# Optimization experiments

Measured on AMD Instinct MI355X. Metric: run time of the kernel, lower is better.

## Reference

```python
import jax, jax.numpy as jnp
from jax import lax
import numpy as np

B, H, W_, C, F = 4, 32, 32, 16, 16
KH, KW = 3, 3
L = 1.0


def setup_inputs() -> dict:
    key = jax.random.key(0)
    k1, k2, k3, k4 = jax.random.split(key, 4)
    inputs = jax.random.normal(k1, (B, H, W_, C), dtype=jnp.float32)
    # lecun_normal-style scales (stddev = 1/sqrt(fan_in))
    m_scale = 1.0 / np.sqrt(H * W_ * 1)
    g_scale = 1.0 / np.sqrt(KH * KW * C)
    M = jax.random.normal(k2, (H, W_, 1, H, W_, 1), dtype=jnp.float32) * m_scale
    Wp = jax.random.normal(k3, (H, W_, 1, H, W_, 1), dtype=jnp.float32) * m_scale
    G = jax.random.normal(k4, (H, W_, KH, KW, C, F), dtype=jnp.float32) * g_scale
    return {"inputs": inputs, "M": M, "Wp": Wp, "G": G}


def reference(inputs, M, Wp, G):
    b, h, w, c = inputs.shape
    kh, kw, f = G.shape[2], G.shape[3], G.shape[5]
    M2 = M[:, :, 0, :, :, 0]   # (i,j,p,q)
    W2 = Wp[:, :, 0, :, :, 0]  # (i,j,p,q)
    # first_term[b,i,j,c] = sum_pq M[i,j,p,q] * inputs[b,p,q,c]
    first = jnp.einsum('ijpq,bpqc->bijc', M2, inputs)
    # One big conv: kernel (kh,kw,c, h*w*f) gives shifted for every output pixel (i,j)
    K = jnp.transpose(G, (2, 3, 4, 0, 1, 5)).reshape(kh, kw, c, h * w * f)
    shifted = lax.conv_general_dilated(
        inputs, K, window_strides=(1, 1), padding='SAME',
        dimension_numbers=('NHWC', 'HWIO', 'NHWC'))
    shifted = shifted.reshape(b, h, w, h, w, f)  # (b,p,q,i,j,f)
    diff = jax.nn.relu(inputs[:, :, :, None, None, :] - shifted)  # (b,p,q,i,j,c)
    # second_term[b,i,j,c] = sum_pq W[i,j,p,q] * relu(inputs - shifted)[b,p,q,i,j,c]
    second = jnp.einsum('ijpq,bpqijc->bijc', W2, diff)
    return first - L * second
```

## Files before the change

### kernel.cpp

```cpp
#include <hip/hip_runtime.h>


typedef __attribute__((ext_vector_type(8))) short bf16x8;
typedef __attribute__((ext_vector_type(4))) float f32x4;

__device__ inline unsigned short f2bf(float x) {
    unsigned u = __float_as_uint(x);
    u += 0x7FFFu + ((u >> 16) & 1u);
    return (unsigned short)(u >> 16);
}
__device__ inline unsigned pack2(float a, float b) {
    return (unsigned)f2bf(a) | ((unsigned)f2bf(b) << 16);
}

__global__ __launch_bounds__(256, 2) void inrf_fused(
    const float* __restrict__ inp,
    const float* __restrict__ M,
    const float* __restrict__ Wp,
    const float* __restrict__ G,
    float* __restrict__ out)
{
    const int bid = blockIdx.x;
    const int g = bid >> 2, b = bid & 3;
    const int t = threadIdx.x, w = t >> 6, l = t & 63;
    const int quad = l >> 4, m = l & 15;
    const int half = quad & 1;

    __shared__ __align__(16) uint4 Xl[1156 * 2];
    __shared__ __align__(16) short Gt[4 * 16 * 168];
    __shared__ float red[4][64];

    for (int i = t; i < 2312; i += 256) Xl[i] = (uint4){0, 0, 0, 0};
    for (int i = t; i < 1536; i += 256) {
        const int ij = i / 384, r2 = i - ij * 384;
        const int cf = r2 / 24, kp = r2 - cf * 24;
        Gt[(ij * 16 + cf) * 168 + 144 + kp] = 0;
    }
    for (int i = t; i < 9216; i += 256) {
        const int ij = i / 2304, r2 = i - ij * 2304;
        const int k = r2 >> 4, cf = r2 & 15;
        Gt[(ij * 16 + cf) * 168 + k] = (short)f2bf(G[g * 9216 + i]);
    }
    __syncthreads();

    {
        const float4* xb = (const float4*)(inp + b * 16384);
        for (int r = t; r < 1024; r += 256) {
            const int p = r >> 5, q = r & 31;
            const int hc = (p + 1) * 34 + (q + 1);
            const float4 f0 = xb[r * 4 + 0], f1 = xb[r * 4 + 1];
            const float4 f2 = xb[r * 4 + 2], f3 = xb[r * 4 + 3];
            uint4 lo, hi;
            lo.x = pack2(f0.x, f0.y); lo.y = pack2(f0.z, f0.w);
            lo.z = pack2(f1.x, f1.y); lo.w = pack2(f1.z, f1.w);
            hi.x = pack2(f2.x, f2.y); hi.y = pack2(f2.z, f2.w);
            hi.z = pack2(f3.x, f3.y); hi.w = pack2(f3.z, f3.w);
            const int sw = hc & 1;
            Xl[2 * hc + sw] = lo;
            Xl[2 * hc + (sw ^ 1)] = hi;
        }
    }

    bf16x8 Bf[4][5];
#pragma unroll
    for (int ij = 0; ij < 4; ++ij)
#pragma unroll
        for (int kk = 0; kk < 5; ++kk)
            Bf[ij][kk] = *(const bf16x8*)&Gt[(ij * 16 + m) * 168 + kk * 32 + quad * 8];

    int K_[5];
#pragma unroll
    for (int kk = 0; kk < 5; ++kk) {
        const int tap = 2 * kk + (quad >> 1);
        const int dh = tap / 3, dw = tap - dh * 3;
        K_[kk] = (dh * 34 + dw) * 32 + ((half ^ (dw & 1)) << 4);
    }
    __syncthreads();

    const int tile0w = w * 16;
    const float* wrow = Wp + g * 4096;
    const float* mrow = M + g * 4096;
    const float* xrow = inp + b * 16384 + m;

    auto loadA = [&](int i, uint4* dst) {
        const int pq = (tile0w + i) * 16 + m;
        const int p = pq >> 5, q = pq & 31;
        const int base = (p * 34 + q) * 32;
        const int qo = (q & 1) << 4;
#pragma unroll
        for (int kk = 0; kk < 5; ++kk) {
            int a = (base + K_[kk]) ^ qo;
            if (kk == 4) a = (quad >= 2) ? 0 : a;
            dst[kk] = *(const uint4*)((const char*)Xl + a);
        }
    };

    float accv[4] = {0.f, 0.f, 0.f, 0.f};
    uint4 Acur[5], Anxt[5];
    loadA(0, Acur);

    for (int i = 0; i < 16; ++i) {
        const int pqb = (tile0w + i) * 16 + quad * 4;

        float4 w2[4], m2[4];
        float xv[4];
#pragma unroll
        for (int ij = 0; ij < 4; ++ij) {
            w2[ij] = *(const float4*)&wrow[ij * 1024 + pqb];
            m2[ij] = *(const float4*)&mrow[ij * 1024 + pqb];
        }
#pragma unroll
        for (int r = 0; r < 4; ++r) xv[r] = xrow[(pqb + r) * 16];

        if (i < 15) loadA(i + 1, Anxt);

        f32x4 C[4];
#pragma unroll
        for (int ij = 0; ij < 4; ++ij) C[ij] = (f32x4){0.f, 0.f, 0.f, 0.f};
#pragma unroll
        for (int kk = 0; kk < 5; ++kk) {
            const bf16x8 a = __builtin_bit_cast(bf16x8, Acur[kk]);
#pragma unroll
            for (int ij = 0; ij < 4; ++ij)
                C[ij] = __builtin_amdgcn_mfma_f32_16x16x32_bf16(a, Bf[ij][kk], C[ij], 0, 0, 0);
        }

#pragma unroll
        for (int ij = 0; ij < 4; ++ij) {
            accv[ij] += m2[ij].x * xv[0] - w2[ij].x * fmaxf(xv[0] - C[ij][0], 0.f);
            accv[ij] += m2[ij].y * xv[1] - w2[ij].y * fmaxf(xv[1] - C[ij][1], 0.f);
            accv[ij] += m2[ij].z * xv[2] - w2[ij].z * fmaxf(xv[2] - C[ij][2], 0.f);
            accv[ij] += m2[ij].w * xv[3] - w2[ij].w * fmaxf(xv[3] - C[ij][3], 0.f);
        }

#pragma unroll
        for (int kk = 0; kk < 5; ++kk) Acur[kk] = Anxt[kk];
    }

#pragma unroll
    for (int ij = 0; ij < 4; ++ij) {
        float v = accv[ij];
        v += __shfl_xor(v, 16);
        v += __shfl_xor(v, 32);
        if (l < 16) red[w][ij * 16 + l] = v;
    }
    __syncthreads();

    if (t < 64) {
        const int oij = t >> 4, oc = t & 15;
        const float r0 = red[0][t] + red[1][t] + red[2][t] + red[3][t];
        out[b * 16384 + (g * 4 + oij) * 16 + oc] = r0;
    }
}

extern "C" void kernel_launch(void* const* d_in, const int* in_sizes, int n_in,
                              void* d_out, int out_size, void* d_ws, size_t ws_size,
                              hipStream_t stream) {
    const float* inp = (const float*)d_in[0];
    const float* M   = (const float*)d_in[1];
    const float* Wp  = (const float*)d_in[2];
    const float* G   = (const float*)d_in[3];
    float* out = (float*)d_out;

    inrf_fused<<<dim3(1024), dim3(256), 0, stream>>>(inp, M, Wp, G, out);
}
```

Baseline: 105.3 us.

## Alias G staging and input tile in one shared buffer to raise occupancy

The separate LDS arrays for the bf16 input halo tile and the transposed G weights are merged into one aliased buffer. G is first written unpadded with coalesced float2 reads and packed to bf16, then gathered into per-thread B fragments with strided short loads. After a barrier the same buffer is zeroed and reused for the input tile. This shrinks LDS per block so launch bounds can ask for 3 blocks per CU, at the cost of extra barriers, bank-conflicted strided fragment gathers and a larger zeroed tile. The zeroed tail also lets the masking select on the last A load be dropped.

Measured after the change: 133.2 us. +26.5%, slower.

```diff
diff --git a/kernel.cpp b/kernel.cpp
--- a/kernel.cpp
+++ b/kernel.cpp
@@ -13,7 +13,7 @@
     return (unsigned)f2bf(a) | ((unsigned)f2bf(b) << 16);
 }
 
-__global__ __launch_bounds__(256, 2) void inrf_fused(
+__global__ __launch_bounds__(256, 3) void inrf_fused(
     const float* __restrict__ inp,
     const float* __restrict__ M,
     const float* __restrict__ Wp,
@@ -26,21 +26,44 @@
     const int quad = l >> 4, m = l & 15;
     const int half = quad & 1;
 
-    __shared__ __align__(16) uint4 Xl[1156 * 2];
-    __shared__ __align__(16) short Gt[4 * 16 * 168];
+    __shared__ __align__(16) char uni[38080];
     __shared__ float red[4][64];
+    uint4*    Xl  = (uint4*)uni;
+    short*    gt  = (short*)uni;
+    unsigned* gtw = (unsigned*)uni;
 
-    for (int i = t; i < 2312; i += 256) Xl[i] = (uint4){0, 0, 0, 0};
-    for (int i = t; i < 1536; i += 256) {
-        const int ij = i / 384, r2 = i - ij * 384;
-        const int cf = r2 / 24, kp = r2 - cf * 24;
-        Gt[(ij * 16 + cf) * 168 + 144 + kp] = 0;
+    {
+        const float* Gs = G + g * 9216;
+        for (int idx = t; idx < 5120; idx += 256) {
+            const int ij = idx / 1280;
+            const int r = (idx - ij * 1280) * 2;
+            unsigned v = 0;
+            if (r < 2304) {
+                const float2 s = *(const float2*)(Gs + ij * 2304 + r);
+                v = pack2(s.x, s.y);
+            }
+            gtw[idx] = v;
+        }
     }
-    for (int i = t; i < 9216; i += 256) {
-        const int ij = i / 2304, r2 = i - ij * 2304;
-        const int k = r2 >> 4, cf = r2 & 15;
-        Gt[(ij * 16 + cf) * 168 + k] = (short)f2bf(G[g * 9216 + i]);
+    __syncthreads();
+
+    bf16x8 Bf[4][5];
+    {
+        const int kq = quad * 8;
+#pragma unroll
+        for (int ij = 0; ij < 4; ++ij)
+#pragma unroll
+            for (int kk = 0; kk < 5; ++kk) {
+                bf16x8 f;
+                const short* s = gt + ij * 2560 + (kk * 32 + kq) * 16 + m;
+#pragma unroll
+                for (int j = 0; j < 8; ++j) f[j] = s[j * 16];
+                Bf[ij][kk] = f;
+            }
     }
+    __syncthreads();
+
+    for (int i = t; i < 2380; i += 256) Xl[i] = (uint4){0, 0, 0, 0};
     __syncthreads();
 
     {
@@ -60,13 +83,6 @@
             Xl[2 * hc + (sw ^ 1)] = hi;
         }
     }
-
-    bf16x8 Bf[4][5];
-#pragma unroll
-    for (int ij = 0; ij < 4; ++ij)
-#pragma unroll
-        for (int kk = 0; kk < 5; ++kk)
-            Bf[ij][kk] = *(const bf16x8*)&Gt[(ij * 16 + m) * 168 + kk * 32 + quad * 8];
 
     int K_[5];
 #pragma unroll
@@ -88,11 +104,8 @@
         const int base = (p * 34 + q) * 32;
         const int qo = (q & 1) << 4;
 #pragma unroll
-        for (int kk = 0; kk < 5; ++kk) {
-            int a = (base + K_[kk]) ^ qo;
-            if (kk == 4) a = (quad >= 2) ? 0 : a;
-            dst[kk] = *(const uint4*)((const char*)Xl + a);
-        }
+        for (int kk = 0; kk < 5; ++kk)
+            dst[kk] = *(const uint4*)((const char*)Xl + ((base + K_[kk]) ^ qo));
     };
 
     float accv[4] = {0.f, 0.f, 0.f, 0.f};
```
